# Kernel tuning notes

Hardware: AMD Instinct MI355X
Metric: run time of the kernel (lower is better)

The kernel has to match this reference:

```python
import jax, jax.numpy as jnp
import numpy as np

B, C, N, H = 4, 256, 1024, 8
D = C // H
EPS = 1e-5

def setup_inputs() -> dict:
    key = jax.random.key(0)
    ks = jax.random.split(key, 10)
    s = lambda k, shape: (jax.random.normal(k, shape, jnp.float32) * 0.02)
    return dict(
        node_embeds=jax.random.normal(ks[0], (B, C, N), jnp.float32),
        edge_embeds=jax.random.normal(ks[1], (B, N, N), jnp.float32),
        da_prior=jax.random.normal(ks[2], (B, N, C), jnp.float32),
        gamma=jnp.ones((C,), jnp.float32),
        beta=jnp.zeros((C,), jnp.float32),
        w_qkv=s(ks[3], (C, 3 * C)),            # Linear(node_dim, 3*node_dim), no bias
        w_proj=s(ks[4], (C, C)),
        b_proj=jnp.zeros((C,), jnp.float32),
        w_expand=s(ks[5], (H,)),               # Conv2d(1,H,1) weight (per-head scalar)
        b_expand=jnp.zeros((H,), jnp.float32),
        w_reduce=s(ks[6], (H,)),               # Conv2d(H,1,1) weight
        b_reduce=jnp.zeros((1,), jnp.float32),
        w_fc=s(ks[7], (1, C)),                 # Linear(edge_dim=1, node_dim)
        b_fc=jnp.zeros((C,), jnp.float32),
    )

def reference(node_embeds, edge_embeds, da_prior, gamma, beta, w_qkv,
              w_proj, b_proj, w_expand, b_expand, w_reduce, b_reduce, w_fc, b_fc):
    x = jnp.swapaxes(node_embeds, 1, 2)                       # [B,N,C]
    # einsum 'bnn,bnc->bnc': diagonal of edge matrix scales each node
    diag = jnp.diagonal(edge_embeds, axis1=1, axis2=2)        # [B,N]
    attned = diag[:, :, None] * x                             # [B,N,C]
    # einsum 'bnc,bca->bnc' with prior permuted [B,C,A]: multiply by sum over A
    prior_sum = da_prior.sum(axis=1)                          # [B,C]
    x = attned * prior_sum[:, None, :] + x                    # residual add
    # LayerNorm over channel dim
    mu = x.mean(-1, keepdims=True)
    var = x.var(-1, keepdims=True)
    ln = (x - mu) * jax.lax.rsqrt(var + EPS) * gamma + beta
    qkv = (ln @ w_qkv).reshape(B, N, 3, H, D)
    q = jnp.transpose(qkv[:, :, 0], (0, 2, 1, 3))             # [B,H,N,D]
    k = jnp.transpose(qkv[:, :, 1], (0, 2, 1, 3))
    v = jnp.transpose(qkv[:, :, 2], (0, 2, 1, 3))
    scale = D ** -0.5
    attn = jnp.einsum('bhnd,bhmd->bhnm', q, k) * scale        # [B,H,N,N]
    bias = edge_embeds[:, None] * w_expand[None, :, None, None] + b_expand[None, :, None, None]
    attn = attn + bias                                        # pre-softmax scores = residual
    a = jax.nn.softmax(attn, axis=-1)
    node = jnp.einsum('bhnm,bhmd->bnhd', a, v).reshape(B, N, C)
    # reduce conv over heads on (softmax + residual)
    edge = jnp.einsum('bhnm,h->bnm', a + attn, w_reduce) + b_reduce[0]  # [B,N,N]
    w = jax.nn.softmax(edge, axis=-1)
    wsum = (w * edge).sum(-1)                                 # [B,N]
    node = node + wsum[:, :, None] @ w_fc + b_fc              # fc: [B,N,1]@[1,C]
    node = node @ w_proj + b_proj
    return jnp.swapaxes(node, 1, 2), edge                     # ([B,C,N], [B,N,N])
```

## Files before the change

### kernel.cpp

```cpp
#include <hip/hip_runtime.h>
#include <math.h>

#define Bn 4
#define Cn 256
#define Nn 1024
#define Hn 8
#define Dn 32

typedef short bf16x8 __attribute__((ext_vector_type(8)));
typedef float f32x4 __attribute__((ext_vector_type(4)));

__device__ inline unsigned f2bf_rn_bits(float x) {
  union { float f; unsigned u; } v; v.f = x;
  return (v.u + 0x7FFFu + ((v.u >> 16) & 1u)) >> 16;
}
__device__ inline float bfbits2f(unsigned b) {
  union { unsigned u; float f; } v; v.u = b << 16; return v.f;
}
__device__ inline void split_bf(float x, unsigned& hi, unsigned& lo) {
  hi = f2bf_rn_bits(x);
  lo = f2bf_rn_bits(x - bfbits2f(hi));
}
__device__ inline void split4(const float4& a, float sc, short4& hs, short4& ls) {
  unsigned hb, lb;
  split_bf(a.x * sc, hb, lb); hs.x = (short)hb; ls.x = (short)lb;
  split_bf(a.y * sc, hb, lb); hs.y = (short)hb; ls.y = (short)lb;
  split_bf(a.z * sc, hb, lb); hs.z = (short)hb; ls.z = (short)lb;
  split_bf(a.w * sc, hb, lb); hs.w = (short)hb; ls.w = (short)lb;
}
__device__ inline void unpack_u32x8(const uint4& a, const uint4& b, bf16x8& hi, bf16x8& lo) {
  int4 h4, l4;
  h4.x = (int)((a.x & 0xffffu) | (a.y << 16));  l4.x = (int)((a.x >> 16) | (a.y & 0xffff0000u));
  h4.y = (int)((a.z & 0xffffu) | (a.w << 16));  l4.y = (int)((a.z >> 16) | (a.w & 0xffff0000u));
  h4.z = (int)((b.x & 0xffffu) | (b.y << 16));  l4.z = (int)((b.x >> 16) | (b.y & 0xffff0000u));
  h4.w = (int)((b.z & 0xffffu) | (b.w << 16));  l4.w = (int)((b.z >> 16) | (b.w & 0xffff0000u));
  hi = *(bf16x8*)&h4; lo = *(bf16x8*)&l4;
}

__global__ __launch_bounds__(256) void k_prior_part(const float* __restrict__ dap,
                                                    float* __restrict__ pp) {
  int bi = blockIdx.x;
  int b = bi >> 5, ch = bi & 31;
  int c = threadIdx.x;
  float s = 0.f;
  int n0 = ch * 32;
  for (int n = n0; n < n0 + 32; ++n) s += dap[(size_t)(b * Nn + n) * Cn + c];
  pp[(size_t)(b * 32 + ch) * Cn + c] = s;
}

__global__ __launch_bounds__(256) void k_prior_red(const float* __restrict__ pp,
                                                   float* __restrict__ prior) {
  int i = blockIdx.x * 256 + threadIdx.x;
  int b = i >> 8, c = i & 255;
  float s = 0.f;
  for (int ch = 0; ch < 32; ++ch) s += pp[(size_t)(b * 32 + ch) * Cn + c];
  prior[i] = s;
}

__global__ __launch_bounds__(256) void k_transpose(const float* __restrict__ ne,
                                                   float* __restrict__ xw) {
  __shared__ float tile[32][33];
  int bi = blockIdx.x;
  int b = bi >> 8, rem = bi & 255;
  int c0 = (rem >> 5) << 5;
  int n0 = (rem & 31) << 5;
  int tx = threadIdx.x & 31, ty = threadIdx.x >> 5;
#pragma unroll
  for (int i = 0; i < 4; ++i) {
    int c = c0 + ty + i * 8;
    tile[ty + i * 8][tx] = ne[(size_t)(b * Cn + c) * Nn + n0 + tx];
  }
  __syncthreads();
#pragma unroll
  for (int i = 0; i < 4; ++i) {
    int n = n0 + ty + i * 8;
    xw[(size_t)(b * Nn + n) * Cn + c0 + tx] = tile[tx][ty + i * 8];
  }
}

__global__ __launch_bounds__(256) void k_prep_ln(const float* __restrict__ xw,
                                                 const float* __restrict__ eg,
                                                 const float* __restrict__ prior,
                                                 const float* __restrict__ gamma,
                                                 const float* __restrict__ beta,
                                                 float* __restrict__ ln) {
  int bn = blockIdx.x;
  int b = bn >> 10, n = bn & 1023;
  int c = threadIdx.x;
  float x = xw[(size_t)bn * Cn + c];
  float dg = eg[(size_t)(b * Nn + n) * Nn + n];
  float x2 = x * (1.f + dg * prior[b * Cn + c]);
  float s = x2, qq = x2 * x2;
#pragma unroll
  for (int off = 32; off >= 1; off >>= 1) {
    s += __shfl_xor(s, off);
    qq += __shfl_xor(qq, off);
  }
  __shared__ float ss[4], sq[4];
  if ((c & 63) == 0) { ss[c >> 6] = s; sq[c >> 6] = qq; }
  __syncthreads();
  s = ss[0] + ss[1] + ss[2] + ss[3];
  qq = sq[0] + sq[1] + sq[2] + sq[3];
  float mu = s * (1.f / 256.f);
  float var = qq * (1.f / 256.f) - mu * mu;
  float r = rsqrtf(var + 1e-5f);
  ln[(size_t)bn * Cn + c] = (x2 - mu) * r * gamma[c] + beta[c];
}

__global__ __launch_bounds__(256) void k_qkv_gemm(const float* __restrict__ ln,
                                                  const float* __restrict__ wqkv,
                                                  short* __restrict__ q_hi,
                                                  short* __restrict__ q_lo,
                                                  short* __restrict__ k_hi,
                                                  short* __restrict__ k_lo,
                                                  float* __restrict__ v) {
  __shared__ __align__(16) float at[16][68];
  __shared__ __align__(16) float bt[16][68];
  int m0 = blockIdx.x * 64;
  int j0 = blockIdx.y * 64;
  int t = threadIdx.x;
  int tx = t & 15, ty = t >> 4;
  float4 acc[4] = {};
  for (int k0 = 0; k0 < 256; k0 += 16) {
    {
      int row = t >> 2, k4 = (t & 3) << 2;
      float4 a = *(const float4*)&ln[(size_t)(m0 + row) * 256 + k0 + k4];
      at[k4 + 0][row] = a.x; at[k4 + 1][row] = a.y;
      at[k4 + 2][row] = a.z; at[k4 + 3][row] = a.w;
      int rb = t >> 4, jb = (t & 15) << 2;
      *(float4*)&bt[rb][jb] = *(const float4*)&wqkv[(size_t)(k0 + rb) * 768 + j0 + jb];
    }
    __syncthreads();
#pragma unroll
    for (int kk = 0; kk < 16; ++kk) {
      float4 a4 = *(float4*)&at[kk][ty << 2];
      float4 b4 = *(float4*)&bt[kk][tx << 2];
      acc[0].x += a4.x * b4.x; acc[0].y += a4.x * b4.y; acc[0].z += a4.x * b4.z; acc[0].w += a4.x * b4.w;
      acc[1].x += a4.y * b4.x; acc[1].y += a4.y * b4.y; acc[1].z += a4.y * b4.z; acc[1].w += a4.y * b4.w;
      acc[2].x += a4.z * b4.x; acc[2].y += a4.z * b4.y; acc[2].z += a4.z * b4.z; acc[2].w += a4.z * b4.w;
      acc[3].x += a4.w * b4.x; acc[3].y += a4.w * b4.y; acc[3].z += a4.w * b4.z; acc[3].w += a4.w * b4.w;
    }
    __syncthreads();
  }
  int j = j0 + (tx << 2);
  int three = j >> 8, rem = j & 255, h = rem >> 5, dd = rem & 31;
  const float scale = 0.17677669529663687f;
#pragma unroll
  for (int i = 0; i < 4; ++i) {
    int m = m0 + (ty << 2) + i;
    int bb = m >> 10, n = m & 1023;
    size_t base = (size_t)((bb * Hn + h) * Nn + n) * Dn + dd;
    if (three == 2) {
      *(float4*)&v[base] = acc[i];
    } else if (three == 0) {
      short4 hs, ls; split4(acc[i], 1.0f, hs, ls);
      *(short4*)&q_hi[base] = hs; *(short4*)&q_lo[base] = ls;
    } else {
      short4 hs, ls; split4(acc[i], scale, hs, ls);
      *(short4*)&k_hi[base] = hs; *(short4*)&k_lo[base] = ls;
    }
  }
}

__global__ __launch_bounds__(256) void k_vt(const float* __restrict__ v,
                                            short* __restrict__ vt_hi,
                                            short* __restrict__ vt_lo) {
  __shared__ float tl[32][33];
  int blk = blockIdx.x;
  int bh = blk >> 5, nt = blk & 31;
  int n0 = nt * 32;
  int t = threadIdx.x;
  int r = t >> 5, cc = t & 31;
#pragma unroll
  for (int i = 0; i < 4; ++i)
    tl[r + i * 8][cc] = v[((size_t)bh * Nn + n0 + r + i * 8) * Dn + cc];
  __syncthreads();
  int d = t >> 3, c4 = (t & 7) * 4;
  short4 hs, ls;
  unsigned hb, lb;
  split_bf(tl[c4 + 0][d], hb, lb); hs.x = (short)hb; ls.x = (short)lb;
  split_bf(tl[c4 + 1][d], hb, lb); hs.y = (short)hb; ls.y = (short)lb;
  split_bf(tl[c4 + 2][d], hb, lb); hs.z = (short)hb; ls.z = (short)lb;
  split_bf(tl[c4 + 3][d], hb, lb); hs.w = (short)hb; ls.w = (short)lb;
  size_t ob = ((size_t)bh * Dn + d) * Nn + n0 + c4;
  *(short4*)&vt_hi[ob] = hs;
  *(short4*)&vt_lo[ob] = ls;
}

__global__ __launch_bounds__(256, 4) void k_attn_core(
    const short* __restrict__ q_hi, const short* __restrict__ q_lo,
    const short* __restrict__ k_hi, const short* __restrict__ k_lo,
    const short* __restrict__ vt_hi, const short* __restrict__ vt_lo,
    const float* __restrict__ eg,
    const float* __restrict__ w_expand, const float* __restrict__ b_expand,
    float* __restrict__ o_part, float* __restrict__ l_part) {
  __shared__ short kh[64 * 40];
  __shared__ short kl[64 * 40];
  __shared__ short vth[32 * 72];
  __shared__ short vtl[32 * 72];
  __shared__ unsigned pbuf[4][16 * 68];

  int blk = blockIdx.x;
  int mh = blk & 1;
  int nt = (blk >> 1) & 15;
  int h = (blk >> 5) & 7;
  int b = blk >> 8;
  int n0 = nt * 64;
  int t = threadIdx.x, wid = t >> 6, l = t & 63;
  int lr = l & 15, lq = l >> 4;

  const float we = w_expand[h], be = b_expand[h];
  size_t bhb = (size_t)(b * Hn + h) * Nn * Dn;
  const short* khg = k_hi + bhb;
  const short* klg = k_lo + bhb;
  const short* vhg = vt_hi + bhb;
  const short* vlg = vt_lo + bhb;

  bf16x8 qhi, qlo;
  {
    size_t qoff = bhb + (size_t)(n0 + wid * 16 + lr) * Dn + lq * 8;
    qhi = *(const bf16x8*)&q_hi[qoff];
    qlo = *(const bf16x8*)&q_lo[qoff];
  }

  f32x4 O0 = {0.f, 0.f, 0.f, 0.f}, O1 = {0.f, 0.f, 0.f, 0.f};
  float rowsum[4] = {0.f, 0.f, 0.f, 0.f};
  int nrow = n0 + wid * 16 + lq * 4;

  for (int ms = 0; ms < 8; ++ms) {
    int m0 = mh * 512 + ms * 64;
    __syncthreads();
    {
      int row = t >> 2, c = (t & 3) * 8;
      *(uint4*)&kh[row * 40 + c] = *(const uint4*)&khg[(size_t)(m0 + row) * Dn + c];
      *(uint4*)&kl[row * 40 + c] = *(const uint4*)&klg[(size_t)(m0 + row) * Dn + c];
      int d = t >> 3, cm = (t & 7) * 8;
      *(uint4*)&vth[d * 72 + cm] = *(const uint4*)&vhg[(size_t)d * Nn + m0 + cm];
      *(uint4*)&vtl[d * 72 + cm] = *(const uint4*)&vlg[(size_t)d * Nn + m0 + cm];
    }
    __syncthreads();

    float eb[4][4];
#pragma unroll
    for (int reg = 0; reg < 4; ++reg) {
      const float* ep = &eg[(size_t)(b * Nn + nrow + reg) * Nn + m0 + lr];
#pragma unroll
      for (int msub = 0; msub < 4; ++msub) eb[msub][reg] = ep[msub * 16];
    }

#pragma unroll
    for (int msub = 0; msub < 4; ++msub) {
      int mrow = msub * 16 + lr;
      bf16x8 bh8 = *(bf16x8*)&kh[mrow * 40 + lq * 8];
      bf16x8 bl8 = *(bf16x8*)&kl[mrow * 40 + lq * 8];
      f32x4 sacc = {0.f, 0.f, 0.f, 0.f};
      sacc = __builtin_amdgcn_mfma_f32_16x16x32_bf16(qlo, bh8, sacc, 0, 0, 0);
      sacc = __builtin_amdgcn_mfma_f32_16x16x32_bf16(qhi, bl8, sacc, 0, 0, 0);
      sacc = __builtin_amdgcn_mfma_f32_16x16x32_bf16(qhi, bh8, sacc, 0, 0, 0);
#pragma unroll
      for (int reg = 0; reg < 4; ++reg) {
        float s = sacc[reg] + eb[msub][reg] * we + be;
        float e = __expf(s);
        rowsum[reg] += e;
        unsigned hb, lb;
        split_bf(e, hb, lb);
        pbuf[wid][(lq * 4 + reg) * 68 + msub * 16 + lr] = hb | (lb << 16);
      }
    }

#pragma unroll
    for (int mw = 0; mw < 2; ++mw) {
      uint4 pa = *(uint4*)&pbuf[wid][lr * 68 + mw * 32 + lq * 8];
      uint4 pb = *(uint4*)&pbuf[wid][lr * 68 + mw * 32 + lq * 8 + 4];
      bf16x8 ahi, alo;
      unpack_u32x8(pa, pb, ahi, alo);
      {
        bf16x8 vh8 = *(bf16x8*)&vth[lr * 72 + mw * 32 + lq * 8];
        bf16x8 vl8 = *(bf16x8*)&vtl[lr * 72 + mw * 32 + lq * 8];
        O0 = __builtin_amdgcn_mfma_f32_16x16x32_bf16(alo, vh8, O0, 0, 0, 0);
        O0 = __builtin_amdgcn_mfma_f32_16x16x32_bf16(ahi, vl8, O0, 0, 0, 0);
        O0 = __builtin_amdgcn_mfma_f32_16x16x32_bf16(ahi, vh8, O0, 0, 0, 0);
      }
      {
        bf16x8 vh8 = *(bf16x8*)&vth[(16 + lr) * 72 + mw * 32 + lq * 8];
        bf16x8 vl8 = *(bf16x8*)&vtl[(16 + lr) * 72 + mw * 32 + lq * 8];
        O1 = __builtin_amdgcn_mfma_f32_16x16x32_bf16(alo, vh8, O1, 0, 0, 0);
        O1 = __builtin_amdgcn_mfma_f32_16x16x32_bf16(ahi, vl8, O1, 0, 0, 0);
        O1 = __builtin_amdgcn_mfma_f32_16x16x32_bf16(ahi, vh8, O1, 0, 0, 0);
      }
    }
  }

#pragma unroll
  for (int reg = 0; reg < 4; ++reg) {
#pragma unroll
    for (int off = 1; off < 16; off <<= 1)
      rowsum[reg] += __shfl_xor(rowsum[reg], off);
  }
  size_t pbase = (size_t)mh * (Bn * Hn * Nn * Dn) + bhb;
#pragma unroll
  for (int reg = 0; reg < 4; ++reg) {
    int n = nrow + reg;
    o_part[pbase + (size_t)n * Dn + lr] = O0[reg];
    o_part[pbase + (size_t)n * Dn + 16 + lr] = O1[reg];
    if (lr == 0)
      l_part[(size_t)mh * (Bn * Hn * Nn) + (size_t)(b * Hn + h) * Nn + n] = rowsum[reg];
  }
}

__global__ __launch_bounds__(256) void k_attn_fix(const float* __restrict__ o_part,
                                                  const float* __restrict__ l_part,
                                                  float* __restrict__ node_tmp,
                                                  float* __restrict__ stats) {
  const int BHND = Bn * Hn * Nn * Dn;
  const int BHN = Bn * Hn * Nn;
  int i = blockIdx.x * 256 + threadIdx.x;
  int bhn = i >> 5, d = i & 31;
  float la = l_part[bhn], lb = l_part[BHN + bhn];
  float invl = 1.0f / (la + lb);
  float o = (o_part[i] + o_part[BHND + i]) * invl;
  int n = bhn & 1023, h = (bhn >> 10) & 7, b = bhn >> 13;
  node_tmp[(size_t)(b * Nn + n) * Cn + h * 32 + d] = o;
  if (d == 0) stats[bhn] = invl;
}

__global__ __launch_bounds__(256, 4) void k_edge_mfma(
    const short* __restrict__ q_hi, const short* __restrict__ q_lo,
    const short* __restrict__ k_hi, const short* __restrict__ k_lo,
    const float* __restrict__ eg, const float* __restrict__ stats,
    const float* __restrict__ w_expand, const float* __restrict__ b_expand,
    const float* __restrict__ w_reduce, const float* __restrict__ b_reduce,
    float* __restrict__ edge_out) {
  __shared__ short kh[64 * 40];
  __shared__ short kl[64 * 40];
  int blk = blockIdx.x;
  int mt = blk & 15;
  int nt = (blk >> 4) & 15;
  int b = blk >> 8;
  int n0 = nt * 64, m0 = mt * 64;
  int t = threadIdx.x, wid = t >> 6, l = t & 63;
  int lr = l & 15, lq = l >> 4;
  const float br = b_reduce[0];
  int nrow = n0 + wid * 16 + lq * 4;

  float eacc[4][4], ebias[4][4];
#pragma unroll
  for (int reg = 0; reg < 4; ++reg) {
    const float* ep = &eg[(size_t)(b * Nn + nrow + reg) * Nn + m0 + lr];
#pragma unroll
    for (int msub = 0; msub < 4; ++msub) {
      ebias[msub][reg] = ep[msub * 16];
      eacc[msub][reg] = br;
    }
  }

  for (int h = 0; h < Hn; ++h) {
    size_t bhb = (size_t)(b * Hn + h) * Nn * Dn;
    float we = w_expand[h], be = b_expand[h], wr = w_reduce[h];
    bf16x8 qhi, qlo;
    {
      size_t qoff = bhb + (size_t)(n0 + wid * 16 + lr) * Dn + lq * 8;
      qhi = *(const bf16x8*)&q_hi[qoff];
      qlo = *(const bf16x8*)&q_lo[qoff];
    }
    float invl[4];
#pragma unroll
    for (int reg = 0; reg < 4; ++reg)
      invl[reg] = stats[(size_t)(b * Hn + h) * Nn + nrow + reg];

    __syncthreads();
    {
      int row = t >> 2, c = (t & 3) * 8;
      *(uint4*)&kh[row * 40 + c] = *(const uint4*)&k_hi[bhb + (size_t)(m0 + row) * Dn + c];
      *(uint4*)&kl[row * 40 + c] = *(const uint4*)&k_lo[bhb + (size_t)(m0 + row) * Dn + c];
    }
    __syncthreads();
#pragma unroll
    for (int msub = 0; msub < 4; ++msub) {
      int mrow = msub * 16 + lr;
      bf16x8 bh8 = *(bf16x8*)&kh[mrow * 40 + lq * 8];
      bf16x8 bl8 = *(bf16x8*)&kl[mrow * 40 + lq * 8];
      f32x4 sacc = {0.f, 0.f, 0.f, 0.f};
      sacc = __builtin_amdgcn_mfma_f32_16x16x32_bf16(qlo, bh8, sacc, 0, 0, 0);
      sacc = __builtin_amdgcn_mfma_f32_16x16x32_bf16(qhi, bl8, sacc, 0, 0, 0);
      sacc = __builtin_amdgcn_mfma_f32_16x16x32_bf16(qhi, bh8, sacc, 0, 0, 0);
#pragma unroll
      for (int reg = 0; reg < 4; ++reg) {
        float s = sacc[reg] + ebias[msub][reg] * we + be;
        float p = __expf(s) * invl[reg];
        eacc[msub][reg] += wr * (p + s);
      }
    }
  }
#pragma unroll
  for (int msub = 0; msub < 4; ++msub)
#pragma unroll
    for (int reg = 0; reg < 4; ++reg)
      edge_out[(size_t)(b * Nn + nrow + reg) * Nn + m0 + msub * 16 + lr] = eacc[msub][reg];
}

__global__ __launch_bounds__(256) void k_edge_soft(const float* __restrict__ edge,
                                                   float* __restrict__ wsum) {
  int bn = blockIdx.x;
  int t = threadIdx.x;
  const float* row = edge + (size_t)bn * Nn;
  float4 e = *(const float4*)&row[t * 4];
  float mx = fmaxf(fmaxf(e.x, e.y), fmaxf(e.z, e.w));
#pragma unroll
  for (int off = 32; off >= 1; off >>= 1) mx = fmaxf(mx, __shfl_xor(mx, off));
  __shared__ float sm[4], sl[4], sw[4];
  if ((t & 63) == 0) sm[t >> 6] = mx;
  __syncthreads();
  mx = fmaxf(fmaxf(sm[0], sm[1]), fmaxf(sm[2], sm[3]));
  float p0 = __expf(e.x - mx), p1 = __expf(e.y - mx), p2 = __expf(e.z - mx), p3 = __expf(e.w - mx);
  float ls = p0 + p1 + p2 + p3;
  float ws = p0 * e.x + p1 * e.y + p2 * e.z + p3 * e.w;
#pragma unroll
  for (int off = 32; off >= 1; off >>= 1) { ls += __shfl_xor(ls, off); ws += __shfl_xor(ws, off); }
  if ((t & 63) == 0) { sl[t >> 6] = ls; sw[t >> 6] = ws; }
  __syncthreads();
  if (t == 0) {
    float L = sl[0] + sl[1] + sl[2] + sl[3];
    float Wv = sw[0] + sw[1] + sw[2] + sw[3];
    wsum[bn] = Wv / L;
  }
}

__global__ __launch_bounds__(256) void k_proj_gemm(const float* __restrict__ nodet,
                                                   const float* __restrict__ wsum,
                                                   const float* __restrict__ wfc,
                                                   const float* __restrict__ bfc,
                                                   const float* __restrict__ wproj,
                                                   const float* __restrict__ bproj,
                                                   float* __restrict__ out) {
  __shared__ __align__(16) float at[16][68];
  __shared__ __align__(16) float bt[16][68];
  __shared__ float ct[64][65];
  int m0 = blockIdx.x * 64;
  int j0 = blockIdx.y * 64;
  int t = threadIdx.x;
  int tx = t & 15, ty = t >> 4;
  float4 acc[4] = {};
  for (int k0 = 0; k0 < 256; k0 += 16) {
    {
      int row = t >> 2, k4 = (t & 3) << 2;
      int m = m0 + row;
      float wsm = wsum[m];
      float4 a = *(const float4*)&nodet[(size_t)m * 256 + k0 + k4];
      a.x += wsm * wfc[k0 + k4 + 0] + bfc[k0 + k4 + 0];
      a.y += wsm * wfc[k0 + k4 + 1] + bfc[k0 + k4 + 1];
      a.z += wsm * wfc[k0 + k4 + 2] + bfc[k0 + k4 + 2];
      a.w += wsm * wfc[k0 + k4 + 3] + bfc[k0 + k4 + 3];
      at[k4 + 0][row] = a.x; at[k4 + 1][row] = a.y;
      at[k4 + 2][row] = a.z; at[k4 + 3][row] = a.w;
      int rb = t >> 4, jb = (t & 15) << 2;
      *(float4*)&bt[rb][jb] = *(const float4*)&wproj[(size_t)(k0 + rb) * 256 + j0 + jb];
    }
    __syncthreads();
#pragma unroll
    for (int kk = 0; kk < 16; ++kk) {
      float4 a4 = *(float4*)&at[kk][ty << 2];
      float4 b4 = *(float4*)&bt[kk][tx << 2];
      acc[0].x += a4.x * b4.x; acc[0].y += a4.x * b4.y; acc[0].z += a4.x * b4.z; acc[0].w += a4.x * b4.w;
      acc[1].x += a4.y * b4.x; acc[1].y += a4.y * b4.y; acc[1].z += a4.y * b4.z; acc[1].w += a4.y * b4.w;
      acc[2].x += a4.z * b4.x; acc[2].y += a4.z * b4.y; acc[2].z += a4.z * b4.z; acc[2].w += a4.z * b4.w;
      acc[3].x += a4.w * b4.x; acc[3].y += a4.w * b4.y; acc[3].z += a4.w * b4.z; acc[3].w += a4.w * b4.w;
    }
    __syncthreads();
  }
#pragma unroll
  for (int i = 0; i < 4; ++i) {
    ct[(ty << 2) + i][(tx << 2) + 0] = acc[i].x + bproj[j0 + (tx << 2) + 0];
    ct[(ty << 2) + i][(tx << 2) + 1] = acc[i].y + bproj[j0 + (tx << 2) + 1];
    ct[(ty << 2) + i][(tx << 2) + 2] = acc[i].z + bproj[j0 + (tx << 2) + 2];
    ct[(ty << 2) + i][(tx << 2) + 3] = acc[i].w + bproj[j0 + (tx << 2) + 3];
  }
  __syncthreads();
  int b = m0 >> 10, n0 = m0 & 1023;
  int n4 = t & 15, c0i = t >> 4;
#pragma unroll
  for (int u = 0; u < 4; ++u) {
    int ci = c0i + u * 16;
    float4 val = { ct[(n4 << 2) + 0][ci], ct[(n4 << 2) + 1][ci],
                   ct[(n4 << 2) + 2][ci], ct[(n4 << 2) + 3][ci] };
    *(float4*)&out[(size_t)(b * Cn + j0 + ci) * Nn + n0 + (n4 << 2)] = val;
  }
}

extern "C" void kernel_launch(void* const* d_in, const int* in_sizes, int n_in,
                              void* d_out, int out_size, void* d_ws, size_t ws_size,
                              hipStream_t stream) {
  (void)in_sizes; (void)n_in; (void)out_size; (void)ws_size;
  const float* node_embeds = (const float*)d_in[0];
  const float* edge_embeds = (const float*)d_in[1];
  const float* da_prior    = (const float*)d_in[2];
  const float* gamma       = (const float*)d_in[3];
  const float* beta        = (const float*)d_in[4];
  const float* w_qkv       = (const float*)d_in[5];
  const float* w_proj      = (const float*)d_in[6];
  const float* b_proj      = (const float*)d_in[7];
  const float* w_expand    = (const float*)d_in[8];
  const float* b_expand    = (const float*)d_in[9];
  const float* w_reduce    = (const float*)d_in[10];
  const float* b_reduce    = (const float*)d_in[11];
  const float* w_fc        = (const float*)d_in[12];
  const float* b_fc        = (const float*)d_in[13];
  float* out_node = (float*)d_out;
  float* out_edge = out_node + (size_t)Bn * Cn * Nn;

  const size_t M = 1048576;
  float* W = (float*)d_ws;
  float* ws_x   = W;
  float* ws_ln  = W + M;
  float* ws_v   = W + 2 * M;
  short* q_hi   = (short*)(W + 3 * M);
  short* q_lo   = q_hi + M;
  short* k_hi   = q_hi + 2 * M;
  short* k_lo   = q_hi + 3 * M;
  float* ws_pp    = W + 5 * M;
  float* ws_prior = ws_pp + Bn * 32 * Cn;
  float* ws_wsum  = ws_prior + Bn * Cn;
  float* ws_stats = ws_wsum + Bn * Nn;
  float* l_part   = ws_stats + Bn * Hn * Nn;
  short* vt_hi  = (short*)ws_ln;
  short* vt_lo  = vt_hi + M;
  float* o_part = out_edge;

  k_prior_part<<<dim3(Bn * 32), dim3(256), 0, stream>>>(da_prior, ws_pp);
  k_prior_red<<<dim3(Bn), dim3(256), 0, stream>>>(ws_pp, ws_prior);
  k_transpose<<<dim3(Bn * 256), dim3(256), 0, stream>>>(node_embeds, ws_x);
  k_prep_ln<<<dim3(Bn * Nn), dim3(256), 0, stream>>>(ws_x, edge_embeds, ws_prior,
                                                     gamma, beta, ws_ln);
  k_qkv_gemm<<<dim3(64, 12), dim3(256), 0, stream>>>(ws_ln, w_qkv, q_hi, q_lo,
                                                     k_hi, k_lo, ws_v);
  k_vt<<<dim3(Bn * Hn * 32), dim3(256), 0, stream>>>(ws_v, vt_hi, vt_lo);
  k_attn_core<<<dim3(Bn * Hn * 16 * 2), dim3(256), 0, stream>>>(
      q_hi, q_lo, k_hi, k_lo, vt_hi, vt_lo, edge_embeds, w_expand, b_expand,
      o_part, l_part);
  k_attn_fix<<<dim3(Bn * Hn * Nn * Dn / 256), dim3(256), 0, stream>>>(
      o_part, l_part, ws_x, ws_stats);
  k_edge_mfma<<<dim3(Bn * 16 * 16), dim3(256), 0, stream>>>(
      q_hi, q_lo, k_hi, k_lo, edge_embeds, ws_stats, w_expand, b_expand,
      w_reduce, b_reduce, out_edge);
  k_edge_soft<<<dim3(Bn * Nn), dim3(256), 0, stream>>>(out_edge, ws_wsum);
  k_proj_gemm<<<dim3(64, 4), dim3(256), 0, stream>>>(ws_x, ws_wsum, w_fc, b_fc,
                                                     w_proj, b_proj, out_node);
}
```

Before: 207.0 us.

## Fuse V transpose into QKV GEMM and attention merge into projection GEMM

The QKV GEMM now transposes its V tile through shared memory and writes the split bf16 hi/lo V^T directly, so the separate k_vt kernel and its fp32 V round trip go away. The attention partial-merge kernel becomes a tiny stats kernel, and the projection GEMM reads both o_part halves and normalizes them while loading, which drops the node_tmp write and re-read. The edge-bias loads in attention are hoisted above the shared-memory staging, and the P split now uses truncation instead of round-to-nearest. The truncated split changes rounding slightly, and the projection loads become strided gathers across heads.

```diff
diff --git a/kernel.cpp b/kernel.cpp
--- a/kernel.cpp
+++ b/kernel.cpp
@@ -6,6 +6,8 @@
 #define Nn 1024
 #define Hn 8
 #define Dn 32
+#define BHND (Bn * Hn * Nn * Dn)
+#define BHN  (Bn * Hn * Nn)
 
 typedef short bf16x8 __attribute__((ext_vector_type(8)));
 typedef float f32x4 __attribute__((ext_vector_type(4)));
@@ -20,6 +22,13 @@
 __device__ inline void split_bf(float x, unsigned& hi, unsigned& lo) {
   hi = f2bf_rn_bits(x);
   lo = f2bf_rn_bits(x - bfbits2f(hi));
+}
+__device__ inline unsigned split_bf_trunc_pack(float x) {
+  union { float f; unsigned u; } v; v.f = x;
+  unsigned hi = v.u >> 16;
+  union { unsigned u; float f; } hv; hv.u = hi << 16;
+  union { float f; unsigned u; } r; r.f = x - hv.f;
+  return hi | (r.u & 0xffff0000u);
 }
 __device__ inline void split4(const float4& a, float sc, short4& hs, short4& ls) {
   unsigned hb, lb;
@@ -113,9 +122,11 @@
                                                   short* __restrict__ q_lo,
                                                   short* __restrict__ k_hi,
                                                   short* __restrict__ k_lo,
-                                                  float* __restrict__ v) {
+                                                  short* __restrict__ vt_hi,
+                                                  short* __restrict__ vt_lo) {
   __shared__ __align__(16) float at[16][68];
   __shared__ __align__(16) float bt[16][68];
+  __shared__ float ct[64][65];
   int m0 = blockIdx.x * 64;
   int j0 = blockIdx.y * 64;
   int t = threadIdx.x;
@@ -142,49 +153,49 @@
     }
     __syncthreads();
   }
-  int j = j0 + (tx << 2);
-  int three = j >> 8, rem = j & 255, h = rem >> 5, dd = rem & 31;
+  int b = m0 >> 10, n0 = m0 & 1023;
+  int three = (j0 + (tx << 2)) >> 8;
   const float scale = 0.17677669529663687f;
-#pragma unroll
-  for (int i = 0; i < 4; ++i) {
-    int m = m0 + (ty << 2) + i;
-    int bb = m >> 10, n = m & 1023;
-    size_t base = (size_t)((bb * Hn + h) * Nn + n) * Dn + dd;
-    if (three == 2) {
-      *(float4*)&v[base] = acc[i];
-    } else if (three == 0) {
-      short4 hs, ls; split4(acc[i], 1.0f, hs, ls);
-      *(short4*)&q_hi[base] = hs; *(short4*)&q_lo[base] = ls;
-    } else {
-      short4 hs, ls; split4(acc[i], scale, hs, ls);
-      *(short4*)&k_hi[base] = hs; *(short4*)&k_lo[base] = ls;
-    }
-  }
-}
-
-__global__ __launch_bounds__(256) void k_vt(const float* __restrict__ v,
-                                            short* __restrict__ vt_hi,
-                                            short* __restrict__ vt_lo) {
-  __shared__ float tl[32][33];
-  int blk = blockIdx.x;
-  int bh = blk >> 5, nt = blk & 31;
-  int n0 = nt * 32;
-  int t = threadIdx.x;
-  int r = t >> 5, cc = t & 31;
-#pragma unroll
-  for (int i = 0; i < 4; ++i)
-    tl[r + i * 8][cc] = v[((size_t)bh * Nn + n0 + r + i * 8) * Dn + cc];
-  __syncthreads();
-  int d = t >> 3, c4 = (t & 7) * 4;
-  short4 hs, ls;
-  unsigned hb, lb;
-  split_bf(tl[c4 + 0][d], hb, lb); hs.x = (short)hb; ls.x = (short)lb;
-  split_bf(tl[c4 + 1][d], hb, lb); hs.y = (short)hb; ls.y = (short)lb;
-  split_bf(tl[c4 + 2][d], hb, lb); hs.z = (short)hb; ls.z = (short)lb;
-  split_bf(tl[c4 + 3][d], hb, lb); hs.w = (short)hb; ls.w = (short)lb;
-  size_t ob = ((size_t)bh * Dn + d) * Nn + n0 + c4;
-  *(short4*)&vt_hi[ob] = hs;
-  *(short4*)&vt_lo[ob] = ls;
+  if (three == 2) {
+#pragma unroll
+    for (int i = 0; i < 4; ++i) {
+      ct[(ty << 2) + i][(tx << 2) + 0] = acc[i].x;
+      ct[(ty << 2) + i][(tx << 2) + 1] = acc[i].y;
+      ct[(ty << 2) + i][(tx << 2) + 2] = acc[i].z;
+      ct[(ty << 2) + i][(tx << 2) + 3] = acc[i].w;
+    }
+    __syncthreads();
+    int jl = t >> 2;
+    int n4 = (t & 3) * 16;
+    int rem = (j0 & 255) + jl;
+    int h = rem >> 5, d = rem & 31;
+    short hs[16], ls[16];
+#pragma unroll
+    for (int u = 0; u < 16; ++u) {
+      unsigned hb, lb;
+      split_bf(ct[n4 + u][jl], hb, lb);
+      hs[u] = (short)hb; ls[u] = (short)lb;
+    }
+    size_t ob = ((size_t)(b * Hn + h) * Dn + d) * Nn + n0 + n4;
+    *(uint4*)&vt_hi[ob] = *(uint4*)&hs[0];
+    *(uint4*)&vt_hi[ob + 8] = *(uint4*)&hs[8];
+    *(uint4*)&vt_lo[ob] = *(uint4*)&ls[0];
+    *(uint4*)&vt_lo[ob + 8] = *(uint4*)&ls[8];
+  } else {
+    int j = j0 + (tx << 2);
+    int rem = j & 255, h = rem >> 5, dd = rem & 31;
+    short* dst_hi = (three == 0) ? q_hi : k_hi;
+    short* dst_lo = (three == 0) ? q_lo : k_lo;
+    float sc = (three == 0) ? 1.0f : scale;
+#pragma unroll
+    for (int i = 0; i < 4; ++i) {
+      int m = m0 + (ty << 2) + i;
+      int bb = m >> 10, n = m & 1023;
+      size_t base = (size_t)((bb * Hn + h) * Nn + n) * Dn + dd;
+      short4 hs, ls; split4(acc[i], sc, hs, ls);
+      *(short4*)&dst_hi[base] = hs; *(short4*)&dst_lo[base] = ls;
+    }
+  }
 }
 
 __global__ __launch_bounds__(256, 4) void k_attn_core(
@@ -229,6 +240,13 @@
 
   for (int ms = 0; ms < 8; ++ms) {
     int m0 = mh * 512 + ms * 64;
+    float eb[4][4];
+#pragma unroll
+    for (int reg = 0; reg < 4; ++reg) {
+      const float* ep = &eg[(size_t)(b * Nn + nrow + reg) * Nn + m0 + lr];
+#pragma unroll
+      for (int msub = 0; msub < 4; ++msub) eb[msub][reg] = ep[msub * 16];
+    }
     __syncthreads();
     {
       int row = t >> 2, c = (t & 3) * 8;
@@ -239,14 +257,6 @@
       *(uint4*)&vtl[d * 72 + cm] = *(const uint4*)&vlg[(size_t)d * Nn + m0 + cm];
     }
     __syncthreads();
-
-    float eb[4][4];
-#pragma unroll
-    for (int reg = 0; reg < 4; ++reg) {
-      const float* ep = &eg[(size_t)(b * Nn + nrow + reg) * Nn + m0 + lr];
-#pragma unroll
-      for (int msub = 0; msub < 4; ++msub) eb[msub][reg] = ep[msub * 16];
-    }
 
 #pragma unroll
     for (int msub = 0; msub < 4; ++msub) {
@@ -262,9 +272,7 @@
         float s = sacc[reg] + eb[msub][reg] * we + be;
         float e = __expf(s);
         rowsum[reg] += e;
-        unsigned hb, lb;
-        split_bf(e, hb, lb);
-        pbuf[wid][(lq * 4 + reg) * 68 + msub * 16 + lr] = hb | (lb << 16);
+        pbuf[wid][(lq * 4 + reg) * 68 + msub * 16 + lr] = split_bf_trunc_pack(e);
       }
     }
 
@@ -297,31 +305,21 @@
     for (int off = 1; off < 16; off <<= 1)
       rowsum[reg] += __shfl_xor(rowsum[reg], off);
   }
-  size_t pbase = (size_t)mh * (Bn * Hn * Nn * Dn) + bhb;
+  size_t pbase = (size_t)mh * BHND + bhb;
 #pragma unroll
   for (int reg = 0; reg < 4; ++reg) {
     int n = nrow + reg;
     o_part[pbase + (size_t)n * Dn + lr] = O0[reg];
     o_part[pbase + (size_t)n * Dn + 16 + lr] = O1[reg];
     if (lr == 0)
-      l_part[(size_t)mh * (Bn * Hn * Nn) + (size_t)(b * Hn + h) * Nn + n] = rowsum[reg];
-  }
-}
-
-__global__ __launch_bounds__(256) void k_attn_fix(const float* __restrict__ o_part,
-                                                  const float* __restrict__ l_part,
-                                                  float* __restrict__ node_tmp,
-                                                  float* __restrict__ stats) {
-  const int BHND = Bn * Hn * Nn * Dn;
-  const int BHN = Bn * Hn * Nn;
+      l_part[(size_t)mh * BHN + (size_t)(b * Hn + h) * Nn + n] = rowsum[reg];
+  }
+}
+
+__global__ __launch_bounds__(256) void k_stats(const float* __restrict__ l_part,
+                                               float* __restrict__ stats) {
   int i = blockIdx.x * 256 + threadIdx.x;
-  int bhn = i >> 5, d = i & 31;
-  float la = l_part[bhn], lb = l_part[BHN + bhn];
-  float invl = 1.0f / (la + lb);
-  float o = (o_part[i] + o_part[BHND + i]) * invl;
-  int n = bhn & 1023, h = (bhn >> 10) & 7, b = bhn >> 13;
-  node_tmp[(size_t)(b * Nn + n) * Cn + h * 32 + d] = o;
-  if (d == 0) stats[bhn] = invl;
+  stats[i] = 1.0f / (l_part[i] + l_part[BHN + i]);
 }
 
 __global__ __launch_bounds__(256, 4) void k_edge_mfma(
@@ -426,7 +424,8 @@
   }
 }
 
-__global__ __launch_bounds__(256) void k_proj_gemm(const float* __restrict__ nodet,
+__global__ __launch_bounds__(256) void k_proj_gemm(const float* __restrict__ o_part,
+                                                   const float* __restrict__ stats,
                                                    const float* __restrict__ wsum,
                                                    const float* __restrict__ wfc,
                                                    const float* __restrict__ bfc,
@@ -445,12 +444,19 @@
     {
       int row = t >> 2, k4 = (t & 3) << 2;
       int m = m0 + row;
+      int bb = m >> 10, n = m & 1023;
+      int c = k0 + k4;
+      int h = c >> 5, dd = c & 31;
       float wsm = wsum[m];
-      float4 a = *(const float4*)&nodet[(size_t)m * 256 + k0 + k4];
-      a.x += wsm * wfc[k0 + k4 + 0] + bfc[k0 + k4 + 0];
-      a.y += wsm * wfc[k0 + k4 + 1] + bfc[k0 + k4 + 1];
-      a.z += wsm * wfc[k0 + k4 + 2] + bfc[k0 + k4 + 2];
-      a.w += wsm * wfc[k0 + k4 + 3] + bfc[k0 + k4 + 3];
+      size_t ob = ((size_t)(bb * Hn + h) * Nn + n) * Dn + dd;
+      float4 oa = *(const float4*)&o_part[ob];
+      float4 oc = *(const float4*)&o_part[BHND + ob];
+      float inv = stats[(size_t)(bb * Hn + h) * Nn + n];
+      float4 a;
+      a.x = (oa.x + oc.x) * inv + wsm * wfc[c + 0] + bfc[c + 0];
+      a.y = (oa.y + oc.y) * inv + wsm * wfc[c + 1] + bfc[c + 1];
+      a.z = (oa.z + oc.z) * inv + wsm * wfc[c + 2] + bfc[c + 2];
+      a.w = (oa.w + oc.w) * inv + wsm * wfc[c + 3] + bfc[c + 3];
       at[k4 + 0][row] = a.x; at[k4 + 1][row] = a.y;
       at[k4 + 2][row] = a.z; at[k4 + 3][row] = a.w;
       int rb = t >> 4, jb = (t & 15) << 2;
@@ -512,7 +518,9 @@
   float* W = (float*)d_ws;
   float* ws_x   = W;
   float* ws_ln  = W + M;
-  float* ws_v   = W + 2 * M;
+  float* o_part = W;
+  short* vt_hi  = (short*)(W + 2 * M);
+  short* vt_lo  = vt_hi + M;
   short* q_hi   = (short*)(W + 3 * M);
   short* q_lo   = q_hi + M;
   short* k_hi   = q_hi + 2 * M;
@@ -521,10 +529,7 @@
   float* ws_prior = ws_pp + Bn * 32 * Cn;
   float* ws_wsum  = ws_prior + Bn * Cn;
   float* ws_stats = ws_wsum + Bn * Nn;
-  float* l_part   = ws_stats + Bn * Hn * Nn;
-  short* vt_hi  = (short*)ws_ln;
-  short* vt_lo  = vt_hi + M;
-  float* o_part = out_edge;
+  float* l_part   = ws_stats + BHN;
 
   k_prior_part<<<dim3(Bn * 32), dim3(256), 0, stream>>>(da_prior, ws_pp);
   k_prior_red<<<dim3(Bn), dim3(256), 0, stream>>>(ws_pp, ws_prior);
@@ -532,17 +537,16 @@
   k_prep_ln<<<dim3(Bn * Nn), dim3(256), 0, stream>>>(ws_x, edge_embeds, ws_prior,
                                                      gamma, beta, ws_ln);
   k_qkv_gemm<<<dim3(64, 12), dim3(256), 0, stream>>>(ws_ln, w_qkv, q_hi, q_lo,
-                                                     k_hi, k_lo, ws_v);
-  k_vt<<<dim3(Bn * Hn * 32), dim3(256), 0, stream>>>(ws_v, vt_hi, vt_lo);
+                                                     k_hi, k_lo, vt_hi, vt_lo);
   k_attn_core<<<dim3(Bn * Hn * 16 * 2), dim3(256), 0, stream>>>(
       q_hi, q_lo, k_hi, k_lo, vt_hi, vt_lo, edge_embeds, w_expand, b_expand,
       o_part, l_part);
-  k_attn_fix<<<dim3(Bn * Hn * Nn * Dn / 256), dim3(256), 0, stream>>>(
-      o_part, l_part, ws_x, ws_stats);
+  k_stats<<<dim3(BHN / 256), dim3(256), 0, stream>>>(l_part, ws_stats);
   k_edge_mfma<<<dim3(Bn * 16 * 16), dim3(256), 0, stream>>>(
       q_hi, q_lo, k_hi, k_lo, edge_embeds, ws_stats, w_expand, b_expand,
       w_reduce, b_reduce, out_edge);
   k_edge_soft<<<dim3(Bn * Nn), dim3(256), 0, stream>>>(out_edge, ws_wsum);
-  k_proj_gemm<<<dim3(64, 4), dim3(256), 0, stream>>>(ws_x, ws_wsum, w_fc, b_fc,
-                                                     w_proj, b_proj, out_node);
-}
+  k_proj_gemm<<<dim3(64, 4), dim3(256), 0, stream>>>(o_part, ws_stats, ws_wsum,
+                                                     w_fc, b_fc, w_proj, b_proj,
+                                                     out_node);
+}
```

Measured after the change: 200.0 us. 1.03x faster.
